# Optimization experiments

Hardware: AMD Instinct MI355X
Metric: run time of the kernel (lower is better)

The kernel has to match this reference:

```python
import jax, jax.numpy as jnp
import numpy as np

# SoftMoE dims: batch B, tokens M, token dim D, experts E, slots P, expert hidden F
B, M, D, E, P, F = 4, 1024, 768, 16, 64, 3072  # P = ceil(M*num_outputs*capacity/E) = 64


def setup_inputs() -> dict:
    key = jax.random.key(0)
    k0, k1, k2, k3 = jax.random.split(key, 4)
    x = jax.random.normal(k0, (B, M, D), jnp.float32)
    # lecun_normal: std = 1/sqrt(fan_in)
    phi = jax.random.normal(k1, (D, E, P), jnp.float32) / np.sqrt(D).astype(np.float32)
    # per-expert 2-layer MLP params (vmap variable_axes={'params':0} -> leading expert axis)
    W1 = jax.random.normal(k2, (E, D, F), jnp.float32) / np.sqrt(D).astype(np.float32)
    b1 = jnp.zeros((E, F), jnp.float32)
    W2 = jax.random.normal(k3, (E, F, D), jnp.float32) / np.sqrt(F).astype(np.float32)
    b2 = jnp.zeros((E, D), jnp.float32)
    return {"x": x, "phi": phi, "W1": W1, "b1": b1, "W2": W2, "b2": b2}


def reference(x, phi, W1, b1, W2, b2):
    # routing logits: [B, M, E, P]
    logits = jnp.einsum('bmd,dnp->bmnp', x, phi)
    # dispatch: softmax over tokens (axis=1)
    dispatch = jax.nn.softmax(logits, axis=1)
    # combine: joint softmax over (experts, slots)
    b_, m_, e_, p_ = logits.shape
    combine = jax.nn.softmax(logits.reshape(b_, m_, e_ * p_), axis=-1).reshape(b_, m_, e_, p_)
    # dispatch tokens into expert slots: [B, E, P, D]
    mix = jnp.nan_to_num(jnp.einsum('bmd,bmnp->bnpd', x, dispatch))
    # per-expert MLP (grouped GEMM over expert axis n), returns (out, hidden)
    hidden = jax.nn.gelu(jnp.einsum('bnpd,ndf->bnpf', mix, W1) + b1[None, :, None, :])
    expert_out = jnp.einsum('bnpf,nfd->bnpd', hidden, W2) + b2[None, :, None, :]
    # combine expert slot outputs back to tokens: [B, M, D]
    outputs = jnp.einsum('bnpd,bmnp->bmd', expert_out, combine)
    probabilities = combine.mean(axis=-1)                      # [B, M, E]
    top_experts = jnp.argmax(probabilities, axis=2, keepdims=True)  # [B, M, 1]
    return outputs, probabilities, top_experts, hidden
```

## Files before the change

kernel.cpp:

```cpp
#include <hip/hip_runtime.h>
#include <hip/hip_bf16.h>


typedef unsigned short u16;
typedef __bf16 bf16x8 __attribute__((ext_vector_type(8)));
typedef float f32x4 __attribute__((ext_vector_type(4)));

__device__ __forceinline__ float gelu_f(float x) {
    const float c = 0.7978845608028654f;
    float u = c * (x + 0.044715f * x * x * x);
    return 0.5f * x * (1.0f + tanhf(u));
}

__device__ __forceinline__ u16 f2b(float x) {
    union { float f; unsigned u; } v; v.f = x;
    unsigned r = v.u + 0x7FFF + ((v.u >> 16) & 1);
    return (u16)(r >> 16);
}

template<bool TRANSA, bool DOGELU>
__global__ __launch_bounds__(256)
void gemm_k(const float* __restrict__ A, const float* __restrict__ Bm,
            const float* __restrict__ bias, float* __restrict__ C,
            int K, int lda, int ldb, int ldc,
            long aZ, long bZ, long cZ, int biasZ,
            long rgsA, long rgsC)
{
    __shared__ float As[16][128];
    __shared__ float Bs[16][64];
    const int z = blockIdx.z;
    A  += (long)z * aZ;
    Bm += (long)z * bZ;
    if (bias) bias += (long)z * biasZ;
    const int row0 = blockIdx.y * 128;
    const int col0 = blockIdx.x * 64;
    const int t  = threadIdx.x;
    const int tx = t & 15;
    const int ty = t >> 4;

    float acc[8][4];
    #pragma unroll
    for (int i = 0; i < 8; ++i)
        #pragma unroll
        for (int j = 0; j < 4; ++j) acc[i][j] = 0.f;

    for (int k0 = 0; k0 < K; k0 += 16) {
        if (TRANSA) {
            const int kk = t >> 5;
            const int ii = (t & 31) * 4;
            const float* pa = A + (long)(k0 + kk) * lda + (row0 + ii);
            float4 v0 = *(const float4*)pa;
            float4 v1 = *(const float4*)(pa + 8L * lda);
            *(float4*)&As[kk][ii]     = v0;
            *(float4*)&As[kk + 8][ii] = v1;
        } else {
            const int ii = t >> 1;
            const int kk = (t & 1) * 8;
            const int grow = row0 + ii;
            const float* pa = A + (long)(grow >> 6) * rgsA
                                + (long)(grow & 63) * lda + (k0 + kk);
            float4 v0 = *(const float4*)pa;
            float4 v1 = *(const float4*)(pa + 4);
            As[kk+0][ii] = v0.x; As[kk+1][ii] = v0.y;
            As[kk+2][ii] = v0.z; As[kk+3][ii] = v0.w;
            As[kk+4][ii] = v1.x; As[kk+5][ii] = v1.y;
            As[kk+6][ii] = v1.z; As[kk+7][ii] = v1.w;
        }
        {
            const int kk = t >> 4;
            const int jj = (t & 15) * 4;
            float4 v = *(const float4*)(Bm + (long)(k0 + kk) * ldb + (col0 + jj));
            *(float4*)&Bs[kk][jj] = v;
        }
        __syncthreads();
        #pragma unroll
        for (int k = 0; k < 16; ++k) {
            float a[8], b[4];
            *(float4*)&a[0] = *(const float4*)&As[k][ty * 8];
            *(float4*)&a[4] = *(const float4*)&As[k][ty * 8 + 4];
            *(float4*)&b[0] = *(const float4*)&Bs[k][tx * 4];
            #pragma unroll
            for (int i = 0; i < 8; ++i)
                #pragma unroll
                for (int j = 0; j < 4; ++j)
                    acc[i][j] = fmaf(a[i], b[j], acc[i][j]);
        }
        __syncthreads();
    }

    float bj[4] = {0.f, 0.f, 0.f, 0.f};
    if (bias) {
        #pragma unroll
        for (int j = 0; j < 4; ++j) bj[j] = bias[col0 + tx * 4 + j];
    }
    #pragma unroll
    for (int i = 0; i < 8; ++i) {
        const int grow = row0 + ty * 8 + i;
        const long rb = (long)(grow >> 6) * rgsC
                      + (long)(grow & 63) * ldc + (col0 + tx * 4);
        float rv[4];
        #pragma unroll
        for (int j = 0; j < 4; ++j) {
            float v = acc[i][j] + bj[j];
            if (DOGELU) v = gelu_f(v);
            rv[j] = v;
        }
        *(float4*)(C + (long)z * cZ + rb) = make_float4(rv[0], rv[1], rv[2], rv[3]);
    }
}

template<bool AF32, bool DOGELU, bool CF32>
__global__ __launch_bounds__(256)
void mfma_gemm(const void* __restrict__ Av, const u16* __restrict__ Bt,
               const float* __restrict__ bias, void* __restrict__ Cv,
               int K, int lda, int ldb, int ldc,
               long aZ, long bZ, long cZ, int biasZ,
               long rgsA, long rgsC)
{
    __shared__ u16 As[128][64];
    __shared__ u16 Bs[128][64];
    const int z    = blockIdx.z;
    const int row0 = blockIdx.y * 128;
    const int col0 = blockIdx.x * 128;
    const int t    = threadIdx.x;
    const int lane = t & 63;
    const int wave = t >> 6;
    const int wr   = (wave >> 1) * 64;
    const int wc   = (wave & 1) * 64;

    const int srow  = t >> 1;
    const int shalf = t & 1;
    const int agrow = row0 + srow;
    const long aRowOff = (long)z * aZ + (long)(agrow >> 6) * rgsA
                       + (long)(agrow & 63) * lda;
    const long bRowOff = (long)z * bZ + (long)(col0 + srow) * ldb;

    f32x4 acc[4][4] = {};

    for (int k0 = 0; k0 < K; k0 += 64) {
        if (AF32) {
            const float* pa = (const float*)Av + aRowOff + k0 + shalf * 32;
            #pragma unroll
            for (int q = 0; q < 4; ++q) {
                float4 u0 = *(const float4*)(pa + q * 8);
                float4 u1 = *(const float4*)(pa + q * 8 + 4);
                u16 tmp[8] = { f2b(u0.x), f2b(u0.y), f2b(u0.z), f2b(u0.w),
                               f2b(u1.x), f2b(u1.y), f2b(u1.z), f2b(u1.w) };
                const int cs = (shalf * 4 + q) ^ (srow & 7);
                *(uint4*)&As[srow][cs * 8] = *(const uint4*)tmp;
            }
        } else {
            const u16* pa = (const u16*)Av + aRowOff + k0 + shalf * 32;
            #pragma unroll
            for (int q = 0; q < 4; ++q) {
                uint4 v = *(const uint4*)(pa + q * 8);
                const int cs = (shalf * 4 + q) ^ (srow & 7);
                *(uint4*)&As[srow][cs * 8] = v;
            }
        }
        {
            const u16* pb = Bt + bRowOff + k0 + shalf * 32;
            #pragma unroll
            for (int q = 0; q < 4; ++q) {
                uint4 v = *(const uint4*)(pb + q * 8);
                const int cs = (shalf * 4 + q) ^ (srow & 7);
                *(uint4*)&Bs[srow][cs * 8] = v;
            }
        }
        __syncthreads();

        #pragma unroll
        for (int kk = 0; kk < 2; ++kk) {
            const int cchunk = kk * 4 + (lane >> 4);
            bf16x8 af[4], bfr[4];
            #pragma unroll
            for (int i = 0; i < 4; ++i) {
                const int m = wr + i * 16 + (lane & 15);
                af[i]  = __builtin_bit_cast(bf16x8,
                           *(const uint4*)&As[m][(cchunk ^ (m & 7)) * 8]);
                const int n = wc + i * 16 + (lane & 15);
                bfr[i] = __builtin_bit_cast(bf16x8,
                           *(const uint4*)&Bs[n][(cchunk ^ (n & 7)) * 8]);
            }
            #pragma unroll
            for (int i = 0; i < 4; ++i)
                #pragma unroll
                for (int j = 0; j < 4; ++j)
                    acc[i][j] = __builtin_amdgcn_mfma_f32_16x16x32_bf16(
                                    af[i], bfr[j], acc[i][j], 0, 0, 0);
        }
        __syncthreads();
    }

    const int cq = lane >> 4;
    #pragma unroll
    for (int j = 0; j < 4; ++j) {
        const int gcol = col0 + wc + j * 16 + (lane & 15);
        const float bv = bias ? bias[(long)z * biasZ + gcol] : 0.f;
        #pragma unroll
        for (int i = 0; i < 4; ++i) {
            #pragma unroll
            for (int r = 0; r < 4; ++r) {
                const int grow = row0 + wr + i * 16 + cq * 4 + r;
                const long co = (long)z * cZ + (long)(grow >> 6) * rgsC
                              + (long)(grow & 63) * ldc + gcol;
                float v = acc[i][j][r] + bv;
                if (DOGELU) v = gelu_f(v);
                if (CF32) ((float*)Cv)[co] = v;
                else      ((u16*)Cv)[co]  = f2b(v);
            }
        }
    }
}

template<bool F32>
__global__ __launch_bounds__(256)
void transpose_k(const void* __restrict__ inV, u16* __restrict__ out, int R, int C)
{
    __shared__ u16 tile[64][72];
    const long zin = (long)blockIdx.z * R * C;
    const int r0 = blockIdx.y * 64, c0 = blockIdx.x * 64;
    const int t  = threadIdx.x;
    const int tr = t >> 4;
    const int tc = (t & 15) * 4;
    #pragma unroll
    for (int p = 0; p < 4; ++p) {
        const int r = tr + p * 16;
        if (F32) {
            float4 v = *(const float4*)((const float*)inV + zin + (long)(r0 + r) * C + c0 + tc);
            tile[r][tc+0] = f2b(v.x); tile[r][tc+1] = f2b(v.y);
            tile[r][tc+2] = f2b(v.z); tile[r][tc+3] = f2b(v.w);
        } else {
            ushort4 v = *(const ushort4*)((const u16*)inV + zin + (long)(r0 + r) * C + c0 + tc);
            tile[r][tc+0] = v.x; tile[r][tc+1] = v.y;
            tile[r][tc+2] = v.z; tile[r][tc+3] = v.w;
        }
    }
    __syncthreads();
    #pragma unroll
    for (int p = 0; p < 4; ++p) {
        const int rr = tr + p * 16;
        ushort4 o;
        o.x = tile[tc+0][rr]; o.y = tile[tc+1][rr];
        o.z = tile[tc+2][rr]; o.w = tile[tc+3][rr];
        *(ushort4*)(out + (long)blockIdx.z * R * C + (long)(c0 + rr) * R + r0 + tc) = o;
    }
}

__global__ __launch_bounds__(1024)
void softmax_m(float* __restrict__ logits)
{
    const int b   = blockIdx.y;
    const int c   = threadIdx.x & 15;
    const int col = blockIdx.x * 16 + c;
    const int mg  = threadIdx.x >> 4;
    float* base = logits + (long)b * 1048576 + col;

    float vals[16];
    float mx = -3.4e38f;
    #pragma unroll
    for (int i = 0; i < 16; ++i) {
        float v = base[(long)(mg * 16 + i) * 1024];
        vals[i] = v;
        mx = fmaxf(mx, v);
    }
    __shared__ float red[64][16];
    red[mg][c] = mx;
    __syncthreads();
    for (int s = 32; s >= 1; s >>= 1) {
        if (mg < s) red[mg][c] = fmaxf(red[mg][c], red[mg + s][c]);
        __syncthreads();
    }
    mx = red[0][c];
    __syncthreads();
    float ssum = 0.f;
    #pragma unroll
    for (int i = 0; i < 16; ++i) { vals[i] = expf(vals[i] - mx); ssum += vals[i]; }
    red[mg][c] = ssum;
    __syncthreads();
    for (int s = 32; s >= 1; s >>= 1) {
        if (mg < s) red[mg][c] += red[mg + s][c];
        __syncthreads();
    }
    const float inv = 1.f / red[0][c];
    #pragma unroll
    for (int i = 0; i < 16; ++i)
        base[(long)(mg * 16 + i) * 1024] = vals[i] * inv;
}

__global__ __launch_bounds__(1024)
void softmax_mT(const float* __restrict__ logits, u16* __restrict__ dispT)
{
    const int b   = blockIdx.y;
    const int c   = threadIdx.x & 15;
    const int col = blockIdx.x * 16 + c;
    const int mg  = threadIdx.x >> 4;
    const float* base = logits + (long)b * 1048576 + col;

    float vals[16];
    float mx = -3.4e38f;
    #pragma unroll
    for (int i = 0; i < 16; ++i) {
        float v = base[(long)(mg * 16 + i) * 1024];
        vals[i] = v;
        mx = fmaxf(mx, v);
    }
    __shared__ float red[64][16];
    red[mg][c] = mx;
    __syncthreads();
    for (int s = 32; s >= 1; s >>= 1) {
        if (mg < s) red[mg][c] = fmaxf(red[mg][c], red[mg + s][c]);
        __syncthreads();
    }
    mx = red[0][c];
    __syncthreads();
    float ssum = 0.f;
    #pragma unroll
    for (int i = 0; i < 16; ++i) { vals[i] = expf(vals[i] - mx); ssum += vals[i]; }
    red[mg][c] = ssum;
    __syncthreads();
    for (int s = 32; s >= 1; s >>= 1) {
        if (mg < s) red[mg][c] += red[mg + s][c];
        __syncthreads();
    }
    const float inv = 1.f / red[0][c];

    union { u16 s[16]; uint4 q[2]; } pk;
    #pragma unroll
    for (int i = 0; i < 16; ++i) pk.s[i] = f2b(vals[i] * inv);
    u16* ob = dispT + (long)b * 1048576 + (long)col * 1024 + mg * 16;
    *(uint4*)ob       = pk.q[0];
    *(uint4*)(ob + 8) = pk.q[1];
}

template<bool B16>
__global__ __launch_bounds__(256)
void softmax_ep(const float* __restrict__ logits, void* __restrict__ comb,
                float* __restrict__ probs, float* __restrict__ tops)
{
    const long r = blockIdx.x;
    const int  t = threadIdx.x;
    const float* row = logits + r * 1024;
    float4 v = *(const float4*)(row + t * 4);

    float mx = fmaxf(fmaxf(v.x, v.y), fmaxf(v.z, v.w));
    #pragma unroll
    for (int s = 32; s; s >>= 1) mx = fmaxf(mx, __shfl_xor(mx, s));
    __shared__ float wr_[4];
    const int wid = t >> 6;
    if ((t & 63) == 0) wr_[wid] = mx;
    __syncthreads();
    mx = fmaxf(fmaxf(wr_[0], wr_[1]), fmaxf(wr_[2], wr_[3]));
    __syncthreads();

    float e0 = expf(v.x - mx), e1 = expf(v.y - mx);
    float e2 = expf(v.z - mx), e3 = expf(v.w - mx);
    float s4 = e0 + e1 + e2 + e3;
    float sm = s4;
    #pragma unroll
    for (int s = 32; s; s >>= 1) sm += __shfl_xor(sm, s);
    if ((t & 63) == 0) wr_[wid] = sm;
    __syncthreads();
    const float tot = wr_[0] + wr_[1] + wr_[2] + wr_[3];
    const float inv = 1.f / tot;

    if (B16) {
        ushort4 o;
        o.x = f2b(e0 * inv); o.y = f2b(e1 * inv);
        o.z = f2b(e2 * inv); o.w = f2b(e3 * inv);
        *(ushort4*)((u16*)comb + r * 1024 + t * 4) = o;
    } else {
        float4 o = make_float4(e0 * inv, e1 * inv, e2 * inv, e3 * inv);
        *(float4*)((float*)comb + r * 1024 + t * 4) = o;
    }

    __shared__ float es[16][16];
    es[t >> 4][t & 15] = s4 * inv;
    __syncthreads();
    __shared__ float pr[16];
    if (t < 16) {
        float ss = 0.f;
        #pragma unroll
        for (int i = 0; i < 16; ++i) ss += es[t][i];
        float p = ss * (1.f / 64.f);
        probs[r * 16 + t] = p;
        pr[t] = p;
    }
    __syncthreads();
    if (t == 0) {
        int best = 0; float bv = pr[0];
        #pragma unroll
        for (int e = 1; e < 16; ++e)
            if (pr[e] > bv) { bv = pr[e]; best = e; }
        tops[r] = (float)best;
    }
}

extern "C" void kernel_launch(void* const* d_in, const int* in_sizes, int n_in,
                              void* d_out, int out_size, void* d_ws, size_t ws_size,
                              hipStream_t stream)
{
    (void)in_sizes; (void)n_in; (void)out_size;
    const float* x   = (const float*)d_in[0];
    const float* phi = (const float*)d_in[1];
    const float* W1  = (const float*)d_in[2];
    const float* b1  = (const float*)d_in[3];
    const float* W2  = (const float*)d_in[4];
    const float* b2  = (const float*)d_in[5];

    float* outputs = (float*)d_out;
    float* probs   = outputs + 3145728;
    float* tops    = outputs + 3145728 + 65536;
    float* hid     = outputs + 3145728 + 65536 + 4096;

    char* wsb = (char*)d_ws;

    if (ws_size >= 209715200ull) {
        float* logits = (float*)(wsb);
        u16*   combB  = (u16*)(wsb + 16777216);
        u16*   dispT  = (u16*)(wsb + 25165824);
        u16*   xT     = (u16*)(wsb + 33554432);
        u16*   mixB   = (u16*)(wsb + 39845888);
        u16*   W1T    = (u16*)(wsb + 46137344);
        u16*   W2T    = (u16*)(wsb + 121634816);
        u16*   eoutN  = (u16*)(wsb + 197132288);
        u16*   eoutT  = (u16*)(wsb + 203423744);

        transpose_k<true><<<dim3(48, 12, 16), 256, 0, stream>>>(W1, W1T, 768, 3072);
        transpose_k<true><<<dim3(12, 48, 16), 256, 0, stream>>>(W2, W2T, 3072, 768);
        transpose_k<true><<<dim3(12, 16, 4),  256, 0, stream>>>(x,  xT,  1024, 768);

        gemm_k<false, false><<<dim3(16, 32, 1), 256, 0, stream>>>(
            x, phi, nullptr, logits,
            768, 768, 1024, 1024, 0L, 0L, 0L, 0, 64L * 768, 64L * 1024);

        softmax_ep<true><<<dim3(4096), 256, 0, stream>>>(logits, combB, probs, tops);
        softmax_mT<<<dim3(64, 4), 1024, 0, stream>>>(logits, dispT);

        mfma_gemm<false, false, false><<<dim3(6, 8, 4), 256, 0, stream>>>(
            dispT, xT, nullptr, mixB,
            1024, 1024, 1024, 768, 1048576L, 786432L, 786432L, 0,
            65536L, 49152L);

        mfma_gemm<false, true, true><<<dim3(24, 2, 16), 256, 0, stream>>>(
            mixB, W1T, b1, hid,
            768, 768, 768, 3072, 49152L, 2359296L, 196608L, 3072,
            786432L, 3145728L);

        mfma_gemm<true, false, false><<<dim3(6, 2, 16), 256, 0, stream>>>(
            hid, W2T, b2, eoutN,
            3072, 3072, 3072, 768, 196608L, 2359296L, 49152L, 768,
            3145728L, 786432L);

        transpose_k<false><<<dim3(12, 16, 4), 256, 0, stream>>>(eoutN, eoutT, 1024, 768);

        mfma_gemm<false, false, true><<<dim3(6, 8, 4), 256, 0, stream>>>(
            combB, eoutT, nullptr, outputs,
            1024, 1024, 1024, 768, 1048576L, 786432L, 786432L, 0,
            65536L, 49152L);
    } else {
        float* logits = (float*)wsb;
        float* comb   = (float*)(wsb + 16777216);
        float* mixb   = (float*)(wsb + 33554432);
        float* eout   = (float*)wsb;

        gemm_k<false, false><<<dim3(16, 32, 1), 256, 0, stream>>>(
            x, phi, nullptr, logits,
            768, 768, 1024, 1024, 0L, 0L, 0L, 0, 64L * 768, 64L * 1024);
        softmax_ep<false><<<dim3(4096), 256, 0, stream>>>(logits, comb, probs, tops);
        softmax_m<<<dim3(64, 4), 1024, 0, stream>>>(logits);
        gemm_k<true, false><<<dim3(12, 8, 4), 256, 0, stream>>>(
            logits, x, nullptr, mixb,
            1024, 1024, 768, 768, 1048576L, 786432L, 786432L, 0, 0L, 64L * 768);
        gemm_k<false, true><<<dim3(48, 2, 16), 256, 0, stream>>>(
            mixb, W1, b1, hid,
            768, 768, 3072, 3072, 49152L, 2359296L, 196608L, 3072,
            786432L, 3145728L);
        gemm_k<false, false><<<dim3(12, 2, 16), 256, 0, stream>>>(
            hid, W2, b2, eout,
            3072, 3072, 768, 768, 196608L, 2359296L, 49152L, 768,
            3145728L, 786432L);
        gemm_k<false, false><<<dim3(12, 8, 4), 256, 0, stream>>>(
            comb, eout, nullptr, outputs,
            1024, 1024, 768, 768, 1048576L, 786432L, 786432L, 0,
            64L * 1024, 64L * 768);
    }
}
```

Measured before the change: 693.1 us.

## Remap GEMM blocks across XCDs and pre-convert hidden to bf16 for W2 GEMM

Flattens the MFMA GEMM grid to 1D and remaps block indices so consecutive logical tiles land on the same XCD (flat&7 interleave), aiming to improve L2 reuse of shared A/B tiles on the chiplet GPU. Adds a separate f32-to-bf16 conversion kernel for the hidden activations, reusing the W1T buffer, so the second expert GEMM reads bf16 instead of converting f32 inside its load loop. This adds an extra kernel launch and a full pass over the hidden tensor, and relies on W1T being dead after the first expert GEMM.

After: 660.5 us. 1.05x faster.

```diff
diff --git a/kernel.cpp b/kernel.cpp
--- a/kernel.cpp
+++ b/kernel.cpp
@@ -115,13 +115,20 @@
                const float* __restrict__ bias, void* __restrict__ Cv,
                int K, int lda, int ldb, int ldc,
                long aZ, long bZ, long cZ, int biasZ,
-               long rgsA, long rgsC)
+               long rgsA, long rgsC, int nbx, int nblk)
 {
     __shared__ u16 As[128][64];
     __shared__ u16 Bs[128][64];
-    const int z    = blockIdx.z;
-    const int row0 = blockIdx.y * 128;
-    const int col0 = blockIdx.x * 128;
+    const int flat = blockIdx.x;
+    const int nper = gridDim.x >> 3;
+    const int r    = (flat & 7) * nper + (flat >> 3);
+    const int z    = r / nblk;
+    const int bi   = r - z * nblk;
+    const int by   = bi / nbx;
+    const int bx   = bi - by * nbx;
+
+    const int row0 = by * 128;
+    const int col0 = bx * 128;
     const int t    = threadIdx.x;
     const int lane = t & 63;
     const int wave = t >> 6;
@@ -200,17 +207,28 @@
         #pragma unroll
         for (int i = 0; i < 4; ++i) {
             #pragma unroll
-            for (int r = 0; r < 4; ++r) {
-                const int grow = row0 + wr + i * 16 + cq * 4 + r;
+            for (int r2 = 0; r2 < 4; ++r2) {
+                const int grow = row0 + wr + i * 16 + cq * 4 + r2;
                 const long co = (long)z * cZ + (long)(grow >> 6) * rgsC
                               + (long)(grow & 63) * ldc + gcol;
-                float v = acc[i][j][r] + bv;
+                float v = acc[i][j][r2] + bv;
                 if (DOGELU) v = gelu_f(v);
                 if (CF32) ((float*)Cv)[co] = v;
                 else      ((u16*)Cv)[co]  = f2b(v);
             }
         }
     }
+}
+
+__global__ __launch_bounds__(256)
+void f32_to_b16(const float* __restrict__ in, u16* __restrict__ out)
+{
+    const long i = ((long)blockIdx.x * 256 + threadIdx.x) * 8;
+    float4 a = *(const float4*)(in + i);
+    float4 b = *(const float4*)(in + i + 4);
+    u16 tmp[8] = { f2b(a.x), f2b(a.y), f2b(a.z), f2b(a.w),
+                   f2b(b.x), f2b(b.y), f2b(b.z), f2b(b.w) };
+    *(uint4*)(out + i) = *(const uint4*)tmp;
 }
 
 template<bool F32>
@@ -425,6 +443,7 @@
         u16*   W2T    = (u16*)(wsb + 121634816);
         u16*   eoutN  = (u16*)(wsb + 197132288);
         u16*   eoutT  = (u16*)(wsb + 203423744);
+        u16*   hidB   = W1T;
 
         transpose_k<true><<<dim3(48, 12, 16), 256, 0, stream>>>(W1, W1T, 768, 3072);
         transpose_k<true><<<dim3(12, 48, 16), 256, 0, stream>>>(W2, W2T, 3072, 768);
@@ -437,27 +456,29 @@
         softmax_ep<true><<<dim3(4096), 256, 0, stream>>>(logits, combB, probs, tops);
         softmax_mT<<<dim3(64, 4), 1024, 0, stream>>>(logits, dispT);
 
-        mfma_gemm<false, false, false><<<dim3(6, 8, 4), 256, 0, stream>>>(
+        mfma_gemm<false, false, false><<<dim3(192), 256, 0, stream>>>(
             dispT, xT, nullptr, mixB,
             1024, 1024, 1024, 768, 1048576L, 786432L, 786432L, 0,
-            65536L, 49152L);
-
-        mfma_gemm<false, true, true><<<dim3(24, 2, 16), 256, 0, stream>>>(
+            65536L, 49152L, 6, 48);
+
+        mfma_gemm<false, true, true><<<dim3(768), 256, 0, stream>>>(
             mixB, W1T, b1, hid,
             768, 768, 768, 3072, 49152L, 2359296L, 196608L, 3072,
-            786432L, 3145728L);
-
-        mfma_gemm<true, false, false><<<dim3(6, 2, 16), 256, 0, stream>>>(
-            hid, W2T, b2, eoutN,
+            786432L, 3145728L, 24, 48);
+
+        f32_to_b16<<<dim3(6144), 256, 0, stream>>>(hid, hidB);
+
+        mfma_gemm<false, false, false><<<dim3(192), 256, 0, stream>>>(
+            hidB, W2T, b2, eoutN,
             3072, 3072, 3072, 768, 196608L, 2359296L, 49152L, 768,
-            3145728L, 786432L);
+            3145728L, 786432L, 6, 12);
 
         transpose_k<false><<<dim3(12, 16, 4), 256, 0, stream>>>(eoutN, eoutT, 1024, 768);
 
-        mfma_gemm<false, false, true><<<dim3(6, 8, 4), 256, 0, stream>>>(
+        mfma_gemm<false, false, true><<<dim3(192), 256, 0, stream>>>(
             combB, eoutT, nullptr, outputs,
             1024, 1024, 1024, 768, 1048576L, 786432L, 786432L, 0,
-            65536L, 49152L);
+            65536L, 49152L, 6, 48);
     } else {
         float* logits = (float*)wsb;
         float* comb   = (float*)(wsb + 16777216);
```
